# Kernel tuning notes

Measured on AMD Instinct MI355X. Metric: run time of the kernel, lower is better.

## Reference

```python
import jax, jax.numpy as jnp
import numpy as np

L, B, N, D, K = 32, 4, 1000, 128, 8


def setup_inputs() -> dict:
    key = jax.random.key(0)
    ks = jax.random.split(key, 10)
    w = lambda k, s: (jax.random.normal(k, s, jnp.float32) * 0.05)
    return {
        "x": jax.random.normal(ks[0], (L, B, N, D), jnp.float32),
        "route_neighbors": jax.random.randint(ks[1], (N, K), 0, N),
        "t_in_w": w(ks[2], (3 * D, D)),
        "t_in_b": w(ks[3], (3 * D,)),
        "t_out_w": w(ks[4], (D, D)),
        "t_out_b": w(ks[5], (D,)),
        "s_in_w": w(ks[6], (3 * D, D)),
        "s_in_b": w(ks[7], (3 * D,)),
        "s_out_w": w(ks[8], (D, D)),
        "s_out_b": w(ks[9], (D,)),
        "n_heads": 8,
    }


def reference(x, route_neighbors, t_in_w, t_in_b, t_out_w, t_out_b,
              s_in_w, s_in_b, s_out_w, s_out_b, n_heads):
    l, b, n, d = x.shape
    h = n_heads
    dh = d // h
    scale = 1.0 / jnp.sqrt(jnp.asarray(dh, x.dtype))

    # ---- temporal MHA: attend over time axis L, batch = (B, N) ----
    wq, wk, wv = jnp.split(t_in_w, 3, axis=0)
    bq, bk, bv = jnp.split(t_in_b, 3, axis=0)
    q = (x @ wq.T + bq).reshape(l, b, n, h, dh)
    k = (x @ wk.T + bk).reshape(l, b, n, h, dh)
    v = (x @ wv.T + bv).reshape(l, b, n, h, dh)
    scores = jnp.einsum('lbnhd,mbnhd->bnhlm', q, k) * scale
    attn = jax.nn.softmax(scores, axis=-1)
    o = jnp.einsum('bnhlm,mbnhd->lbnhd', attn, v).reshape(l, b, n, d)
    t_out = o @ t_out_w.T + t_out_b

    # ---- spatial MHA: per node, single-token query over K gathered neighbors ----
    swq, swk, swv = jnp.split(s_in_w, 3, axis=0)
    sbq, sbk, sbv = jnp.split(s_in_b, 3, axis=0)
    xn = x[:, :, route_neighbors]                         # (L,B,N,K,D) gather
    sq = (x @ swq.T + sbq).reshape(l, b, n, h, dh)
    sk = (xn @ swk.T + sbk).reshape(l, b, n, -1, h, dh)
    sv = (xn @ swv.T + sbv).reshape(l, b, n, -1, h, dh)
    s_scores = jnp.einsum('lbnhd,lbnkhd->lbnhk', sq, sk) * scale
    s_attn = jax.nn.softmax(s_scores, axis=-1)
    so = jnp.einsum('lbnhk,lbnkhd->lbnhd', s_attn, sv).reshape(l, b, n, d)
    s_out = so @ s_out_w.T + s_out_b

    return t_out + s_out
```

## Files before the change

### kernel.cpp

```cpp
#include <hip/hip_runtime.h>
#include <math.h>

#define L_ 32
#define B_ 4
#define N_ 1000
#define D_ 128
#define H_ 8
#define DH_ 16
#define KN_ 8
#define M_ (L_ * B_ * N_)

typedef __attribute__((ext_vector_type(8))) short short8;
typedef __attribute__((ext_vector_type(8))) unsigned short ushort8v;
typedef __attribute__((ext_vector_type(4))) float floatx4;
typedef __attribute__((ext_vector_type(4))) unsigned uintx4;

static __device__ __forceinline__ unsigned short f2bf(float f) {
  union { float f; unsigned u; } v; v.f = f;
  unsigned r = v.u + 0x7fffu + ((v.u >> 16) & 1u);
  return (unsigned short)(r >> 16);
}
static __device__ __forceinline__ float bf2f(unsigned short s) {
  union { unsigned u; float f; } v; v.u = ((unsigned)s) << 16;
  return v.f;
}
static __device__ __forceinline__ unsigned cvtpk(float lo, float hi) {
  unsigned r;
  asm("v_cvt_pk_bf16_f32 %0, %1, %2" : "=v"(r) : "v"(lo), "v"(hi));
  return r;
}
static __device__ __forceinline__ float vexp2(float x) {
  float r; asm("v_exp_f32 %0, %1" : "=v"(r) : "v"(x)); return r;
}
static __device__ __forceinline__ float vrcp(float x) {
  float r; asm("v_rcp_f32 %0, %1" : "=v"(r) : "v"(x)); return r;
}
union B8 { uintx4 u; short8 s; };
union BW8 { uintx4 u; ushort8v s; };
static __device__ __forceinline__ void gload_lds16(const unsigned short* g,
                                                   unsigned short* l) {
  __builtin_amdgcn_global_load_lds(
      (const __attribute__((address_space(1))) unsigned int*)g,
      (__attribute__((address_space(3))) unsigned int*)l, 16, 0, 0);
}

__global__ __launch_bounds__(256) void prep_kernel(
    const float* __restrict__ x, const float* __restrict__ wt_in,
    const float* __restrict__ ws_in, const float* __restrict__ wt_out,
    const float* __restrict__ ws_out, unsigned short* __restrict__ ximg,
    unsigned short* __restrict__ wimg) {
  const int bid = blockIdx.x, t = threadIdx.x;
  const float* src;
  unsigned short* dst;
  if (bid < 1000) {
    src = x + (size_t)bid * 16384;
    dst = ximg + (size_t)bid * 16384;
  } else {
    int w = bid - 1000;
    if (w < 3) src = wt_in + (size_t)w * 16384;
    else if (w < 6) src = ws_in + (size_t)(w - 3) * 16384;
    else if (w == 6) src = wt_out;
    else src = ws_out;
    dst = wimg + (size_t)w * 16384;
  }
#pragma unroll
  for (int it = 0; it < 8; ++it) {
    int gi = it * 256 + t;
    int m = gi >> 4, g = gi & 15;
    const float4* sp = (const float4*)(src + m * 128 + g * 8);
    float4 a = sp[0], b = sp[1];
    ushort8v o;
    o[0] = f2bf(a.x); o[1] = f2bf(a.y); o[2] = f2bf(a.z); o[3] = f2bf(a.w);
    o[4] = f2bf(b.x); o[5] = f2bf(b.y); o[6] = f2bf(b.z); o[7] = f2bf(b.w);
    *(ushort8v*)(dst + (size_t)(m * 16 + (g ^ (m & 7))) * 8) = o;
  }
}

__global__ __launch_bounds__(256) void proj_mfma(
    const unsigned short* __restrict__ ximg,
    const unsigned short* __restrict__ wimg, const float* __restrict__ bias,
    unsigned short* __restrict__ out) {
  __shared__ unsigned short As[128 * 128];
  __shared__ unsigned short Bs[128 * 128];
  const int t = threadIdx.x;
  const int bm = blockIdx.x / 3, bn = blockIdx.x % 3;
  const unsigned short* aSrc = ximg + (size_t)bm * 16384;
  const unsigned short* bSrc = wimg + (size_t)bn * 16384;
#pragma unroll
  for (int it = 0; it < 8; ++it) {
    int gi = it * 256 + t;
    gload_lds16(aSrc + (size_t)gi * 8, &As[gi * 8]);
    gload_lds16(bSrc + (size_t)gi * 8, &Bs[gi * 8]);
  }
  __syncthreads();
  const int wave = t >> 6, lane = t & 63;
  const int wm = (wave >> 1) * 64, wn = (wave & 1) * 64;
  const int lq = lane >> 4, l16 = lane & 15;
  floatx4 acc[4][4] = {};
#pragma unroll
  for (int kk = 0; kk < 4; ++kk) {
    int g = kk * 4 + lq;
    short8 a[4], b[4];
#pragma unroll
    for (int i = 0; i < 4; ++i) {
      int ma = wm + i * 16 + l16;
      a[i] = *(const short8*)(&As[(ma * 16 + (g ^ (ma & 7))) * 8]);
      int nb = wn + i * 16 + l16;
      b[i] = *(const short8*)(&Bs[(nb * 16 + (g ^ (nb & 7))) * 8]);
    }
#pragma unroll
    for (int i = 0; i < 4; ++i)
#pragma unroll
      for (int j = 0; j < 4; ++j)
        acc[i][j] = __builtin_amdgcn_mfma_f32_16x16x32_bf16(a[i], b[j],
                                                            acc[i][j], 0, 0, 0);
  }
  const size_t rowBase = (size_t)bm * 128 + wm;
  const int colBase = bn * 128 + wn;
#pragma unroll
  for (int j = 0; j < 4; ++j) {
    float bb = bias[colBase + j * 16 + l16];
#pragma unroll
    for (int i = 0; i < 4; ++i) {
#pragma unroll
      for (int r = 0; r < 4; ++r) {
        size_t row = rowBase + i * 16 + lq * 4 + r;
        out[row * 384 + colBase + j * 16 + l16] = f2bf(acc[i][j][r] + bb);
      }
    }
  }
}

__global__ __launch_bounds__(256) void tattn_fused(
    const unsigned short* __restrict__ ximg,
    const unsigned short* __restrict__ wimg,
    const float* __restrict__ bias,
    unsigned short* __restrict__ oimg) {
  __shared__ unsigned short Sx[512 * 8];
  __shared__ unsigned short Sqk[4][2][32 * 40];
  const int t = threadIdx.x;
  const int b = blockIdx.x / N_;
  const int n = blockIdx.x % N_;
  const int c = b * N_ + n;
#pragma unroll
  for (int it = 0; it < 2; ++it) {
    const int s = it * 256 + t;
    const int ml = s >> 4, gs = s & 15;
    const int G = gs ^ (ml & 7);
    const size_t rg = (size_t)ml * (B_ * N_) + c;
    gload_lds16(ximg + (rg >> 7) * 16384 +
                    ((rg & 127) * 16 + (size_t)(G ^ ((int)rg & 7))) * 8,
                &Sx[s * 8]);
  }
  asm volatile("s_waitcnt vmcnt(0)" ::: "memory");
  __syncthreads();

  const int wv = t >> 6, lane = t & 63;
  const int lq = lane >> 4, l16 = lane & 15;

  floatx4 aQ[2][2] = {}, aK[2][2] = {}, aV[2][2] = {};
#pragma unroll
  for (int kk = 0; kk < 4; ++kk) {
    short8 a[2];
#pragma unroll
    for (int i = 0; i < 2; ++i) {
      const int ml = i * 16 + l16;
      a[i] = *(const short8*)&Sx[(ml * 16 + ((kk * 4 + lq) ^ (ml & 7))) * 8];
    }
#pragma unroll
    for (int mat = 0; mat < 3; ++mat) {
      const unsigned short* wb = wimg + mat * 16384;
      short8 bf[2];
#pragma unroll
      for (int j = 0; j < 2; ++j) {
        const int nb = wv * 32 + j * 16 + l16;
        bf[j] =
            *(const short8*)&wb[(nb * 16 + ((kk * 4 + lq) ^ (nb & 7))) * 8];
      }
#pragma unroll
      for (int i = 0; i < 2; ++i)
#pragma unroll
        for (int j = 0; j < 2; ++j) {
          floatx4* acc = mat == 0 ? &aQ[i][j] : (mat == 1 ? &aK[i][j] : &aV[i][j]);
          *acc = __builtin_amdgcn_mfma_f32_16x16x32_bf16(a[i], bf[j], *acc, 0,
                                                         0, 0);
        }
    }
  }
  const float bQ0 = bias[wv * 32 + l16], bQ1 = bias[wv * 32 + 16 + l16];
  const float bK0 = bias[128 + wv * 32 + l16],
              bK1 = bias[128 + wv * 32 + 16 + l16];
  const float bV0 = bias[256 + wv * 32 + l16],
              bV1 = bias[256 + wv * 32 + 16 + l16];
  unsigned short* Sq = Sqk[wv][0];
  unsigned short* Sk = Sqk[wv][1];
#pragma unroll
  for (int i = 0; i < 2; ++i)
#pragma unroll
    for (int j = 0; j < 2; ++j) {
      const float qb_ = j ? bQ1 : bQ0, kb_ = j ? bK1 : bK0;
      const unsigned q01 = cvtpk(aQ[i][j][0] + qb_, aQ[i][j][1] + qb_);
      const unsigned q23 = cvtpk(aQ[i][j][2] + qb_, aQ[i][j][3] + qb_);
      const unsigned k01 = cvtpk(aK[i][j][0] + kb_, aK[i][j][1] + kb_);
      const unsigned k23 = cvtpk(aK[i][j][2] + kb_, aK[i][j][3] + kb_);
      unsigned short* q_ = &Sq[(i * 16 + lq * 4) * 40 + j * 16 + l16];
      unsigned short* k_ = &Sk[(i * 16 + lq * 4) * 40 + j * 16 + l16];
      q_[0] = (unsigned short)q01;   q_[40] = (unsigned short)(q01 >> 16);
      q_[80] = (unsigned short)q23;  q_[120] = (unsigned short)(q23 >> 16);
      k_[0] = (unsigned short)k01;   k_[40] = (unsigned short)(k01 >> 16);
      k_[80] = (unsigned short)k23;  k_[120] = (unsigned short)(k23 >> 16);
    }
  unsigned short* ob[8];
  int rsw[8];
#pragma unroll
  for (int lt = 0; lt < 2; ++lt)
#pragma unroll
    for (int r = 0; r < 4; ++r) {
      const int l = lt * 16 + lq * 4 + r;
      const size_t rg = (size_t)l * (B_ * N_) + c;
      ob[lt * 4 + r] = oimg + (rg >> 7) * 16384 + (size_t)(rg & 127) * 128;
      rsw[lt * 4 + r] = (int)(rg & 7);
    }

  const float CSC = 0.25f * 1.4426950408889634f;
#pragma unroll
  for (int hh = 0; hh < 2; ++hh) {
    const int h = wv * 2 + hh;
    short8 ka0 = {}, ka1 = {}, qb0 = {}, qb1 = {};
    if (lq < 2) {
      const int go = (2 * hh + lq) * 8;
      ka0 = *(const short8*)&Sk[l16 * 40 + go];
      ka1 = *(const short8*)&Sk[(16 + l16) * 40 + go];
      qb0 = *(const short8*)&Sq[l16 * 40 + go];
      qb1 = *(const short8*)&Sq[(16 + l16) * 40 + go];
    }
    floatx4 st00 = {}, st01 = {}, st10 = {}, st11 = {};
    st00 = __builtin_amdgcn_mfma_f32_16x16x32_bf16(ka0, qb0, st00, 0, 0, 0);
    st01 = __builtin_amdgcn_mfma_f32_16x16x32_bf16(ka0, qb1, st01, 0, 0, 0);
    st10 = __builtin_amdgcn_mfma_f32_16x16x32_bf16(ka1, qb0, st10, 0, 0, 0);
    st11 = __builtin_amdgcn_mfma_f32_16x16x32_bf16(ka1, qb1, st11, 0, 0, 0);
    const float bV = hh ? bV1 : bV0;
    B8 vu;
    vu.u[0] = cvtpk(aV[0][hh][0] + bV, aV[0][hh][1] + bV);
    vu.u[1] = cvtpk(aV[0][hh][2] + bV, aV[0][hh][3] + bV);
    vu.u[2] = cvtpk(aV[1][hh][0] + bV, aV[1][hh][1] + bV);
    vu.u[3] = cvtpk(aV[1][hh][2] + bV, aV[1][hh][3] + bV);
    const short8 vb = vu.s;
    short8 pa0, pa1;
    {
      floatx4 a = st00 * CSC, cc = st10 * CSC;
      float mx = fmaxf(fmaxf(fmaxf(a[0], a[1]), fmaxf(a[2], a[3])),
                       fmaxf(fmaxf(cc[0], cc[1]), fmaxf(cc[2], cc[3])));
      mx = fmaxf(mx, __shfl_xor(mx, 16));
      mx = fmaxf(mx, __shfl_xor(mx, 32));
      float p0 = vexp2(a[0] - mx), p1 = vexp2(a[1] - mx);
      float p2 = vexp2(a[2] - mx), p3 = vexp2(a[3] - mx);
      float p4 = vexp2(cc[0] - mx), p5 = vexp2(cc[1] - mx);
      float p6 = vexp2(cc[2] - mx), p7 = vexp2(cc[3] - mx);
      float sm = ((p0 + p1) + (p2 + p3)) + ((p4 + p5) + (p6 + p7));
      sm += __shfl_xor(sm, 16);
      sm += __shfl_xor(sm, 32);
      const float inv = vrcp(sm);
      B8 pu;
      pu.u[0] = cvtpk(p0 * inv, p1 * inv);
      pu.u[1] = cvtpk(p2 * inv, p3 * inv);
      pu.u[2] = cvtpk(p4 * inv, p5 * inv);
      pu.u[3] = cvtpk(p6 * inv, p7 * inv);
      pa0 = pu.s;
    }
    {
      floatx4 a = st01 * CSC, cc = st11 * CSC;
      float mx = fmaxf(fmaxf(fmaxf(a[0], a[1]), fmaxf(a[2], a[3])),
                       fmaxf(fmaxf(cc[0], cc[1]), fmaxf(cc[2], cc[3])));
      mx = fmaxf(mx, __shfl_xor(mx, 16));
      mx = fmaxf(mx, __shfl_xor(mx, 32));
      float p0 = vexp2(a[0] - mx), p1 = vexp2(a[1] - mx);
      float p2 = vexp2(a[2] - mx), p3 = vexp2(a[3] - mx);
      float p4 = vexp2(cc[0] - mx), p5 = vexp2(cc[1] - mx);
      float p6 = vexp2(cc[2] - mx), p7 = vexp2(cc[3] - mx);
      float sm = ((p0 + p1) + (p2 + p3)) + ((p4 + p5) + (p6 + p7));
      sm += __shfl_xor(sm, 16);
      sm += __shfl_xor(sm, 32);
      const float inv = vrcp(sm);
      B8 pu;
      pu.u[0] = cvtpk(p0 * inv, p1 * inv);
      pu.u[1] = cvtpk(p2 * inv, p3 * inv);
      pu.u[2] = cvtpk(p4 * inv, p5 * inv);
      pu.u[3] = cvtpk(p6 * inv, p7 * inv);
      pa1 = pu.s;
    }
    floatx4 o0 = {}, o1 = {};
    o0 = __builtin_amdgcn_mfma_f32_16x16x32_bf16(pa0, vb, o0, 0, 0, 0);
    o1 = __builtin_amdgcn_mfma_f32_16x16x32_bf16(pa1, vb, o1, 0, 0, 0);
    const int d = h * 16 + l16;
    const int gd = d >> 3, de = d & 7;
#pragma unroll
    for (int r = 0; r < 4; ++r) {
      const unsigned w = cvtpk(o0[r], o1[r]);
      ob[r][(gd ^ rsw[r]) * 8 + de] = (unsigned short)w;
      ob[4 + r][(gd ^ rsw[4 + r]) * 8 + de] = (unsigned short)(w >> 16);
    }
  }
}

__global__ __launch_bounds__(512) void sattn_final(
    const unsigned short* __restrict__ qkv, const int* __restrict__ route,
    const unsigned short* __restrict__ otimg,
    const unsigned short* __restrict__ wtimg,
    const unsigned short* __restrict__ wsimg,
    const float* __restrict__ bt, const float* __restrict__ bs,
    float* __restrict__ out) {
  __shared__ unsigned short Os[128 * 128];
  const int t = threadIdx.x;
  const int bb = blockIdx.x;
  const int bm = (bb & 7) * 125 + (bb >> 3);
  const int h = t & 7;
#pragma unroll
  for (int it2 = 0; it2 < 2; ++it2) {
    const int rl = (t >> 3) + it2 * 64;
    const int gr = bm * 128 + rl;
    const int lb = (int)((unsigned)gr / 1000u);
    const int n = gr - lb * 1000;
    float q[16];
    {
      const unsigned short* qp = qkv + (size_t)gr * 384 + h * DH_;
      ushort8v q0 = *(const ushort8v*)qp;
      ushort8v q1 = *(const ushort8v*)(qp + 8);
#pragma unroll
      for (int i = 0; i < 8; ++i) { q[i] = bf2f(q0[i]); q[8 + i] = bf2f(q1[i]); }
    }
    int nb[KN_];
#pragma unroll
    for (int kk = 0; kk < KN_; ++kk) nb[kk] = route[n * KN_ + kk];
    ushort8v kr[KN_][2], vr[KN_][2];
#pragma unroll
    for (int kk = 0; kk < KN_; ++kk) {
      const unsigned short* base = qkv + ((size_t)lb * N_ + nb[kk]) * 384;
      const unsigned short* kp = base + 128 + h * DH_;
      const unsigned short* vp = base + 256 + h * DH_;
      kr[kk][0] = *(const ushort8v*)kp;
      kr[kk][1] = *(const ushort8v*)(kp + 8);
      vr[kk][0] = *(const ushort8v*)vp;
      vr[kk][1] = *(const ushort8v*)(vp + 8);
    }
    float sc[KN_];
    float mx = -1e30f;
#pragma unroll
    for (int kk = 0; kk < KN_; ++kk) {
      float d = 0.f;
#pragma unroll
      for (int i = 0; i < 8; ++i) {
        d = fmaf(q[i], bf2f(kr[kk][0][i]), d);
        d = fmaf(q[8 + i], bf2f(kr[kk][1][i]), d);
      }
      d *= 0.25f;
      sc[kk] = d;
      mx = fmaxf(mx, d);
    }
    float ssum = 0.f;
#pragma unroll
    for (int kk = 0; kk < KN_; ++kk) { sc[kk] = __expf(sc[kk] - mx); ssum += sc[kk]; }
    float inv = 1.f / ssum;
    float oa[16];
#pragma unroll
    for (int i = 0; i < 16; ++i) oa[i] = 0.f;
#pragma unroll
    for (int kk = 0; kk < KN_; ++kk) {
      float p = sc[kk] * inv;
#pragma unroll
      for (int i = 0; i < 8; ++i) {
        oa[i] = fmaf(p, bf2f(vr[kk][0][i]), oa[i]);
        oa[8 + i] = fmaf(p, bf2f(vr[kk][1][i]), oa[8 + i]);
      }
    }
    BW8 w0, w1;
    w0.u[0] = cvtpk(oa[0], oa[1]);   w0.u[1] = cvtpk(oa[2], oa[3]);
    w0.u[2] = cvtpk(oa[4], oa[5]);   w0.u[3] = cvtpk(oa[6], oa[7]);
    w1.u[0] = cvtpk(oa[8], oa[9]);   w1.u[1] = cvtpk(oa[10], oa[11]);
    w1.u[2] = cvtpk(oa[12], oa[13]); w1.u[3] = cvtpk(oa[14], oa[15]);
    const int sw = rl & 7;
    *(ushort8v*)(&Os[(size_t)(rl * 16 + ((2 * h) ^ sw)) * 8]) = w0.s;
    *(ushort8v*)(&Os[(size_t)(rl * 16 + ((2 * h + 1) ^ sw)) * 8]) = w1.s;
  }
  __syncthreads();

  const int wave = t >> 6, lane = t & 63;
  const int wm = (wave >> 2) * 64, wn = (wave & 3) * 32;
  const int lq = lane >> 4, l16 = lane & 15;
  floatx4 acc[4][2] = {};
#pragma unroll
  for (int p = 0; p < 2; ++p) {
    if (p) {
      __syncthreads();
#pragma unroll
      for (int it = 0; it < 4; ++it) {
        int gi = it * 512 + t;
        gload_lds16(otimg + (size_t)bm * 16384 + (size_t)gi * 8, &Os[gi * 8]);
      }
      asm volatile("s_waitcnt vmcnt(0)" ::: "memory");
      __syncthreads();
    }
    const unsigned short* wsrc = p ? wtimg : wsimg;
#pragma unroll
    for (int kk = 0; kk < 4; ++kk) {
      int g = kk * 4 + lq;
      short8 a[4], b[2];
#pragma unroll
      for (int i = 0; i < 4; ++i) {
        int ma = wm + i * 16 + l16;
        a[i] = *(const short8*)(&Os[(ma * 16 + (g ^ (ma & 7))) * 8]);
      }
#pragma unroll
      for (int j = 0; j < 2; ++j) {
        int nb2 = wn + j * 16 + l16;
        b[j] = *(const short8*)(&wsrc[(nb2 * 16 + (g ^ (nb2 & 7))) * 8]);
      }
#pragma unroll
      for (int i = 0; i < 4; ++i)
#pragma unroll
        for (int j = 0; j < 2; ++j)
          acc[i][j] = __builtin_amdgcn_mfma_f32_16x16x32_bf16(a[i], b[j],
                                                              acc[i][j], 0, 0, 0);
    }
  }
  const size_t rowBase = (size_t)bm * 128 + wm;
#pragma unroll
  for (int j = 0; j < 2; ++j) {
    int col = wn + j * 16 + l16;
    float bb2 = bt[col] + bs[col];
#pragma unroll
    for (int i = 0; i < 4; ++i) {
#pragma unroll
      for (int r = 0; r < 4; ++r) {
        size_t row = rowBase + i * 16 + lq * 4 + r;
        out[row * 128 + col] = acc[i][j][r] + bb2;
      }
    }
  }
}

extern "C" void kernel_launch(void* const* d_in, const int* in_sizes, int n_in,
                              void* d_out, int out_size, void* d_ws,
                              size_t ws_size, hipStream_t stream) {
  const float* x = (const float*)d_in[0];
  const int* route = (const int*)d_in[1];
  const float* t_in_w = (const float*)d_in[2];
  const float* t_in_b = (const float*)d_in[3];
  const float* t_out_w = (const float*)d_in[4];
  const float* t_out_b = (const float*)d_in[5];
  const float* s_in_w = (const float*)d_in[6];
  const float* s_in_b = (const float*)d_in[7];
  const float* s_out_w = (const float*)d_in[8];
  const float* s_out_b = (const float*)d_in[9];
  float* out = (float*)d_out;
  unsigned short* ximg = (unsigned short*)d_ws;
  unsigned short* qkv = ximg + (size_t)M_ * 128;
  unsigned short* o_t = qkv + (size_t)M_ * 384;
  unsigned short* wimg = o_t + (size_t)M_ * 128;

  prep_kernel<<<1008, 256, 0, stream>>>(x, t_in_w, s_in_w, t_out_w, s_out_w,
                                        ximg, wimg);
  tattn_fused<<<B_ * N_, 256, 0, stream>>>(ximg, wimg, t_in_b, o_t);
  proj_mfma<<<(M_ / 128) * 3, 256, 0, stream>>>(ximg, wimg + 3 * 16384,
                                                s_in_b, qkv);
  sattn_final<<<M_ / 128, 512, 0, stream>>>(qkv, route, o_t,
                                            wimg + 6 * 16384, wimg + 7 * 16384,
                                            t_out_b, s_out_b, out);
}
```

Measured before the change: 257.6 us.

## Fuse x conversion and spatial QKV projection into temporal attention kernel

The standalone x-to-bf16 conversion pass and the separate spatial QKV projection GEMM are removed. The temporal attention kernel now reads fp32 x directly, converts it into LDS, and reuses that tile to compute the spatial q/k/v projection for its 32 rows. This drops the ximg write/read round trip and one kernel launch. In exchange, the fused kernel does more work per block with more accumulator registers, and writes the qkv output as scattered 2-byte stores with a large row stride.

```diff
diff --git a/kernel.cpp b/kernel.cpp
--- a/kernel.cpp
+++ b/kernel.cpp
@@ -44,25 +44,17 @@
       (__attribute__((address_space(3))) unsigned int*)l, 16, 0, 0);
 }
 
-__global__ __launch_bounds__(256) void prep_kernel(
-    const float* __restrict__ x, const float* __restrict__ wt_in,
-    const float* __restrict__ ws_in, const float* __restrict__ wt_out,
-    const float* __restrict__ ws_out, unsigned short* __restrict__ ximg,
+__global__ __launch_bounds__(256) void prep_w(
+    const float* __restrict__ wt_in, const float* __restrict__ ws_in,
+    const float* __restrict__ wt_out, const float* __restrict__ ws_out,
     unsigned short* __restrict__ wimg) {
-  const int bid = blockIdx.x, t = threadIdx.x;
+  const int w = blockIdx.x, t = threadIdx.x;
   const float* src;
-  unsigned short* dst;
-  if (bid < 1000) {
-    src = x + (size_t)bid * 16384;
-    dst = ximg + (size_t)bid * 16384;
-  } else {
-    int w = bid - 1000;
-    if (w < 3) src = wt_in + (size_t)w * 16384;
-    else if (w < 6) src = ws_in + (size_t)(w - 3) * 16384;
-    else if (w == 6) src = wt_out;
-    else src = ws_out;
-    dst = wimg + (size_t)w * 16384;
-  }
+  if (w < 3) src = wt_in + (size_t)w * 16384;
+  else if (w < 6) src = ws_in + (size_t)(w - 3) * 16384;
+  else if (w == 6) src = wt_out;
+  else src = ws_out;
+  unsigned short* dst = wimg + (size_t)w * 16384;
 #pragma unroll
   for (int it = 0; it < 8; ++it) {
     int gi = it * 256 + t;
@@ -76,65 +68,12 @@
   }
 }
 
-__global__ __launch_bounds__(256) void proj_mfma(
-    const unsigned short* __restrict__ ximg,
-    const unsigned short* __restrict__ wimg, const float* __restrict__ bias,
-    unsigned short* __restrict__ out) {
-  __shared__ unsigned short As[128 * 128];
-  __shared__ unsigned short Bs[128 * 128];
-  const int t = threadIdx.x;
-  const int bm = blockIdx.x / 3, bn = blockIdx.x % 3;
-  const unsigned short* aSrc = ximg + (size_t)bm * 16384;
-  const unsigned short* bSrc = wimg + (size_t)bn * 16384;
-#pragma unroll
-  for (int it = 0; it < 8; ++it) {
-    int gi = it * 256 + t;
-    gload_lds16(aSrc + (size_t)gi * 8, &As[gi * 8]);
-    gload_lds16(bSrc + (size_t)gi * 8, &Bs[gi * 8]);
-  }
-  __syncthreads();
-  const int wave = t >> 6, lane = t & 63;
-  const int wm = (wave >> 1) * 64, wn = (wave & 1) * 64;
-  const int lq = lane >> 4, l16 = lane & 15;
-  floatx4 acc[4][4] = {};
-#pragma unroll
-  for (int kk = 0; kk < 4; ++kk) {
-    int g = kk * 4 + lq;
-    short8 a[4], b[4];
-#pragma unroll
-    for (int i = 0; i < 4; ++i) {
-      int ma = wm + i * 16 + l16;
-      a[i] = *(const short8*)(&As[(ma * 16 + (g ^ (ma & 7))) * 8]);
-      int nb = wn + i * 16 + l16;
-      b[i] = *(const short8*)(&Bs[(nb * 16 + (g ^ (nb & 7))) * 8]);
-    }
-#pragma unroll
-    for (int i = 0; i < 4; ++i)
-#pragma unroll
-      for (int j = 0; j < 4; ++j)
-        acc[i][j] = __builtin_amdgcn_mfma_f32_16x16x32_bf16(a[i], b[j],
-                                                            acc[i][j], 0, 0, 0);
-  }
-  const size_t rowBase = (size_t)bm * 128 + wm;
-  const int colBase = bn * 128 + wn;
-#pragma unroll
-  for (int j = 0; j < 4; ++j) {
-    float bb = bias[colBase + j * 16 + l16];
-#pragma unroll
-    for (int i = 0; i < 4; ++i) {
-#pragma unroll
-      for (int r = 0; r < 4; ++r) {
-        size_t row = rowBase + i * 16 + lq * 4 + r;
-        out[row * 384 + colBase + j * 16 + l16] = f2bf(acc[i][j][r] + bb);
-      }
-    }
-  }
-}
-
-__global__ __launch_bounds__(256) void tattn_fused(
-    const unsigned short* __restrict__ ximg,
+__global__ __launch_bounds__(256) void tattn_sproj(
+    const float* __restrict__ x,
     const unsigned short* __restrict__ wimg,
-    const float* __restrict__ bias,
+    const float* __restrict__ bt_in,
+    const float* __restrict__ bs_in,
+    unsigned short* __restrict__ qkv,
     unsigned short* __restrict__ oimg) {
   __shared__ unsigned short Sx[512 * 8];
   __shared__ unsigned short Sqk[4][2][32 * 40];
@@ -142,17 +81,20 @@
   const int b = blockIdx.x / N_;
   const int n = blockIdx.x % N_;
   const int c = b * N_ + n;
-#pragma unroll
-  for (int it = 0; it < 2; ++it) {
-    const int s = it * 256 + t;
-    const int ml = s >> 4, gs = s & 15;
-    const int G = gs ^ (ml & 7);
-    const size_t rg = (size_t)ml * (B_ * N_) + c;
-    gload_lds16(ximg + (rg >> 7) * 16384 +
-                    ((rg & 127) * 16 + (size_t)(G ^ ((int)rg & 7))) * 8,
-                &Sx[s * 8]);
-  }
-  asm volatile("s_waitcnt vmcnt(0)" ::: "memory");
+  {
+    const int ml = t >> 3, s2 = t & 7;
+    const float4* sp =
+        (const float4*)(x + ((size_t)ml * (B_ * N_) + c) * 128 + s2 * 16);
+    float4 a0 = sp[0], a1 = sp[1], a2 = sp[2], a3 = sp[3];
+    BW8 o0, o1;
+    o0.u[0] = cvtpk(a0.x, a0.y); o0.u[1] = cvtpk(a0.z, a0.w);
+    o0.u[2] = cvtpk(a1.x, a1.y); o0.u[3] = cvtpk(a1.z, a1.w);
+    o1.u[0] = cvtpk(a2.x, a2.y); o1.u[1] = cvtpk(a2.z, a2.w);
+    o1.u[2] = cvtpk(a3.x, a3.y); o1.u[3] = cvtpk(a3.z, a3.w);
+    const int g0 = 2 * s2;
+    *(ushort8v*)&Sx[(ml * 16 + (g0 ^ (ml & 7))) * 8] = o0.s;
+    *(ushort8v*)&Sx[(ml * 16 + ((g0 + 1) ^ (ml & 7))) * 8] = o1.s;
+  }
   __syncthreads();
 
   const int wv = t >> 6, lane = t & 63;
@@ -187,11 +129,11 @@
         }
     }
   }
-  const float bQ0 = bias[wv * 32 + l16], bQ1 = bias[wv * 32 + 16 + l16];
-  const float bK0 = bias[128 + wv * 32 + l16],
-              bK1 = bias[128 + wv * 32 + 16 + l16];
-  const float bV0 = bias[256 + wv * 32 + l16],
-              bV1 = bias[256 + wv * 32 + 16 + l16];
+  const float bQ0 = bt_in[wv * 32 + l16], bQ1 = bt_in[wv * 32 + 16 + l16];
+  const float bK0 = bt_in[128 + wv * 32 + l16],
+              bK1 = bt_in[128 + wv * 32 + 16 + l16];
+  const float bV0 = bt_in[256 + wv * 32 + l16],
+              bV1 = bt_in[256 + wv * 32 + 16 + l16];
   unsigned short* Sq = Sqk[wv][0];
   unsigned short* Sk = Sqk[wv][1];
 #pragma unroll
@@ -301,6 +243,45 @@
       ob[4 + r][(gd ^ rsw[4 + r]) * 8 + de] = (unsigned short)(w >> 16);
     }
   }
+
+  floatx4 accs[2][6] = {};
+#pragma unroll
+  for (int kk = 0; kk < 4; ++kk) {
+    const int g = kk * 4 + lq;
+    short8 a[2];
+#pragma unroll
+    for (int i = 0; i < 2; ++i) {
+      const int ml = i * 16 + l16;
+      a[i] = *(const short8*)&Sx[(ml * 16 + (g ^ (ml & 7))) * 8];
+    }
+#pragma unroll
+    for (int q = 0; q < 6; ++q) {
+      const int cb = wv * 6 + q;
+      const unsigned short* wb = wimg + (size_t)(3 + (cb >> 3)) * 16384;
+      const int nbt = (cb & 7) * 16 + l16;
+      const short8 bf =
+          *(const short8*)&wb[(nbt * 16 + (g ^ (nbt & 7))) * 8];
+      accs[0][q] =
+          __builtin_amdgcn_mfma_f32_16x16x32_bf16(a[0], bf, accs[0][q], 0, 0, 0);
+      accs[1][q] =
+          __builtin_amdgcn_mfma_f32_16x16x32_bf16(a[1], bf, accs[1][q], 0, 0, 0);
+    }
+  }
+#pragma unroll
+  for (int q = 0; q < 6; ++q) {
+    const int col = (wv * 6 + q) * 16 + l16;
+    const float bb = bs_in[col];
+#pragma unroll
+    for (int i = 0; i < 2; ++i) {
+      const unsigned u01 = cvtpk(accs[i][q][0] + bb, accs[i][q][1] + bb);
+      const unsigned u23 = cvtpk(accs[i][q][2] + bb, accs[i][q][3] + bb);
+      const size_t r0 = ((size_t)(i * 16 + lq * 4) * (B_ * N_) + c) * 384 + col;
+      qkv[r0] = (unsigned short)u01;
+      qkv[r0 + (size_t)(B_ * N_) * 384] = (unsigned short)(u01 >> 16);
+      qkv[r0 + (size_t)2 * (B_ * N_) * 384] = (unsigned short)u23;
+      qkv[r0 + (size_t)3 * (B_ * N_) * 384] = (unsigned short)(u23 >> 16);
+    }
+  }
 }
 
 __global__ __launch_bounds__(512) void sattn_final(
@@ -453,16 +434,12 @@
   const float* s_out_w = (const float*)d_in[8];
   const float* s_out_b = (const float*)d_in[9];
   float* out = (float*)d_out;
-  unsigned short* ximg = (unsigned short*)d_ws;
-  unsigned short* qkv = ximg + (size_t)M_ * 128;
+  unsigned short* qkv = (unsigned short*)d_ws;
   unsigned short* o_t = qkv + (size_t)M_ * 384;
   unsigned short* wimg = o_t + (size_t)M_ * 128;
 
-  prep_kernel<<<1008, 256, 0, stream>>>(x, t_in_w, s_in_w, t_out_w, s_out_w,
-                                        ximg, wimg);
-  tattn_fused<<<B_ * N_, 256, 0, stream>>>(ximg, wimg, t_in_b, o_t);
-  proj_mfma<<<(M_ / 128) * 3, 256, 0, stream>>>(ximg, wimg + 3 * 16384,
-                                                s_in_b, qkv);
+  prep_w<<<8, 256, 0, stream>>>(t_in_w, s_in_w, t_out_w, s_out_w, wimg);
+  tattn_sproj<<<B_ * N_, 256, 0, stream>>>(x, wimg, t_in_b, s_in_b, qkv, o_t);
   sattn_final<<<M_ / 128, 512, 0, stream>>>(qkv, route, o_t,
                                             wimg + 6 * 16384, wimg + 7 * 16384,
                                             t_out_b, s_out_b, out);
```

Result: faster. 248.3 us (-3.6%).
